# Performance work log

Measured on AMD Instinct MI355X. Metric: run time of the kernel, lower is better.

The kernel has to match this reference:

```python
import jax, jax.numpy as jnp
import numpy as np
from jax import lax

# ---- static config (matches init_kwargs) ----
B, D, H, HD, MLP = 64, 768, 12, 64, 3072
DEPTH = 11                     # trunk blocks; block 12 is used (twice) as b1/b2
IMG_H, IMG_W, P, S = 256, 128, 16, 12
NY, NX = (IMG_H - P) // S + 1, (IMG_W - P) // S + 1   # 21, 10
NP = NY * NX                   # 210 patches
N = NP + 1                     # +CLS = 211 tokens
NUM_CIDS = 8
SCALE = HD ** -0.5
SIE = 3.0                      # sie_xishu
SHIFT, GROUPS, DIV = 5, 2, 4
EPS = 1e-6
_PNAMES = ["ln1_g", "ln1_b", "qkv_w", "qkv_b", "proj_w", "proj_b",
           "ln2_g", "ln2_b", "fc1_w", "fc1_b", "fc2_w", "fc2_b"]


def layernorm(x, g, b):
    m = jnp.mean(x, -1, keepdims=True)
    v = jnp.mean(jnp.square(x - m), -1, keepdims=True)
    return (x - m) * lax.rsqrt(v + EPS) * g + b


def block(x, p):
    """Pre-norm ViT block: manual attention (q@k.T softmax @v) + GELU MLP."""
    ln1g, ln1b, qkvw, qkvb, projw, projb, ln2g, ln2b, fc1w, fc1b, fc2w, fc2b = p
    Bn, Nn = x.shape[0], x.shape[1]
    h = layernorm(x, ln1g, ln1b)
    qkv = (h @ qkvw + qkvb).reshape(Bn, Nn, 3, H, HD)
    q, k, v = qkv[:, :, 0], qkv[:, :, 1], qkv[:, :, 2]           # [B,N,H,HD]
    attn = jax.nn.softmax(jnp.einsum('bnhd,bmhd->bhnm', q * SCALE, k), axis=-1)
    o = jnp.einsum('bhnm,bmhd->bnhd', attn, v).reshape(Bn, Nn, D)
    x = x + o @ projw + projb
    h = layernorm(x, ln2g, ln2b)
    return x + jax.nn.gelu(h @ fc1w + fc1b, approximate=False) @ fc2w + fc2b


def _block_params(k, lead=()):
    ks = jax.random.split(k, 4)
    z = lambda s: jnp.zeros(lead + s, jnp.float32)
    o = lambda s: jnp.ones(lead + s, jnp.float32)
    r = lambda kk, s, fan: jax.random.normal(kk, lead + s, jnp.float32) * (fan ** -0.5)
    return dict(ln1_g=o((D,)), ln1_b=z((D,)),
                qkv_w=r(ks[0], (D, 3 * D), D), qkv_b=z((3 * D,)),
                proj_w=r(ks[1], (D, D), D), proj_b=z((D,)),
                ln2_g=o((D,)), ln2_b=z((D,)),
                fc1_w=r(ks[2], (D, MLP), D), fc1_b=z((MLP,)),
                fc2_w=r(ks[3], (MLP, D), MLP), fc2_b=z((D,)))


def setup_inputs() -> dict:
    key = jax.random.key(0)
    k = jax.random.split(key, 8)
    inp = {
        "x": jax.random.normal(k[0], (B, 3, IMG_H, IMG_W), jnp.float32),
        "cids": jax.random.randint(k[1], (B,), 0, NUM_CIDS),
        "conv_w": jax.random.normal(k[2], (D, 3, P, P), jnp.float32) * np.float32(np.sqrt(2.0 / (P * P * D))),
        "conv_b": jnp.zeros((D,), jnp.float32),
        "cls_token": jax.random.normal(k[3], (1, 1, D), jnp.float32) * 0.02,
        "pos_embed": jax.random.normal(k[4], (1, N, D), jnp.float32) * 0.02,
        "sie_embed": jax.random.normal(k[5], (NUM_CIDS, 1, D), jnp.float32) * 0.02,
    }
    for name, arr in _block_params(k[6], (DEPTH,)).items():
        inp["blk_" + name] = arr
    for pre, kk in (("b1_", jax.random.fold_in(key, 101)), ("b2_", jax.random.fold_in(key, 102))):
        for name, arr in _block_params(kk).items():
            inp[pre + name] = arr
        inp[pre + "norm_g"] = jnp.ones((D,), jnp.float32)
        inp[pre + "norm_b"] = jnp.zeros((D,), jnp.float32)
    return inp


def reference(x, cids, conv_w, conv_b, cls_token, pos_embed, sie_embed,
              blk_ln1_g, blk_ln1_b, blk_qkv_w, blk_qkv_b, blk_proj_w, blk_proj_b,
              blk_ln2_g, blk_ln2_b, blk_fc1_w, blk_fc1_b, blk_fc2_w, blk_fc2_b,
              b1_ln1_g, b1_ln1_b, b1_qkv_w, b1_qkv_b, b1_proj_w, b1_proj_b,
              b1_ln2_g, b1_ln2_b, b1_fc1_w, b1_fc1_b, b1_fc2_w, b1_fc2_b,
              b1_norm_g, b1_norm_b,
              b2_ln1_g, b2_ln1_b, b2_qkv_w, b2_qkv_b, b2_proj_w, b2_proj_b,
              b2_ln2_g, b2_ln2_b, b2_fc1_w, b2_fc1_b, b2_fc2_w, b2_fc2_b,
              b2_norm_g, b2_norm_b):
    Bn = x.shape[0]
    # overlapping patch embed: Conv2d(3->768, k=16, s=12), flatten, transpose
    y = lax.conv_general_dilated(x, conv_w, (S, S), 'VALID',
                                 dimension_numbers=('NCHW', 'OIHW', 'NCHW'))
    y = (y + conv_b[None, :, None, None]).reshape(Bn, D, NP).transpose(0, 2, 1)
    t = jnp.concatenate([jnp.broadcast_to(cls_token, (Bn, 1, D)), y], axis=1)
    t = t + pos_embed + SIE * sie_embed[cids]   # SIE camera embedding
    # 11 trunk blocks via scan over stacked params
    stk = (blk_ln1_g, blk_ln1_b, blk_qkv_w, blk_qkv_b, blk_proj_w, blk_proj_b,
           blk_ln2_g, blk_ln2_b, blk_fc1_w, blk_fc1_b, blk_fc2_w, blk_fc2_b)
    t = lax.scan(lambda c, p: (block(c, p), None), t, stk)[0]
    # global branch: b1 = block12 + final norm, take CLS
    b1p = (b1_ln1_g, b1_ln1_b, b1_qkv_w, b1_qkv_b, b1_proj_w, b1_proj_b,
           b1_ln2_g, b1_ln2_b, b1_fc1_w, b1_fc1_b, b1_fc2_w, b1_fc2_b)
    f0 = layernorm(block(t, b1p), b1_norm_g, b1_norm_b)[:, 0]
    # shuffle_unit(t, shift=5, group=2, begin=1) -> jigsaw rearranged patches [B,210,D]
    xs = jnp.concatenate([t[:, SHIFT:], t[:, 1:SHIFT]], axis=1)
    xs = xs.reshape(Bn, GROUPS, -1, D).transpose(0, 2, 1, 3).reshape(Bn, -1, D)
    token = t[:, 0:1]
    pl = NP // DIV                                   # 52
    b2p = (b2_ln1_g, b2_ln1_b, b2_qkv_w, b2_qkv_b, b2_proj_w, b2_proj_b,
           b2_ln2_g, b2_ln2_b, b2_fc1_w, b2_fc1_b, b2_fc2_w, b2_fc2_b)
    feats = [f0]
    for i in range(DIV):
        seg = jnp.concatenate([token, xs[:, i * pl:(i + 1) * pl]], axis=1)   # [B,53,D]
        feats.append(layernorm(block(seg, b2p), b2_norm_g, b2_norm_b)[:, 0])
    # eval output with neck_feat='before': necks pass features through;
    # concat global + local/divide_length -> [B, 5*768]
    return jnp.concatenate([feats[0]] + [f / DIV for f in feats[1:]], axis=1)
```

## Files before the change

kernel.cpp:

```cpp
#include <hip/hip_runtime.h>
#include <hip/hip_bf16.h>
#include <cstdint>
#include <cstddef>
#include <math.h>

using bf16 = __hip_bfloat16;
typedef __bf16 bf16x8 __attribute__((ext_vector_type(8)));
typedef float f32x4 __attribute__((ext_vector_type(4)));

static constexpr int NHEAD = 12;
static constexpr int NTOK  = 211;
static constexpr int DEPTH = 11;

static __device__ __forceinline__ void gload_lds16(const bf16* g, bf16* lds) {
  __builtin_amdgcn_global_load_lds(
      (const __attribute__((address_space(1))) uint32_t*)g,
      (__attribute__((address_space(3))) uint32_t*)lds,
      16, 0, 0);
}

__device__ __forceinline__ float gelu_f(float x) {
  float u = x * (0.7978845608f + 0.0356774081f * x * x);
  float t = 1.f - 2.f / (__expf(2.f * u) + 1.f);
  return 0.5f * x * (1.f + t);
}

static __device__ __forceinline__ unsigned short bf16_bits(float x) {
  return __builtin_bit_cast(unsigned short, __float2bfloat16(x));
}

template <bool GELU, bool RES, typename CT, int OUT>
__global__ __launch_bounds__(256) void gemm_db(
    const bf16* __restrict__ A, const bf16* __restrict__ Bt,
    const float* __restrict__ bias, const float* __restrict__ res,
    CT* __restrict__ C, int M, int N, int K, int gn, int sA, int sR, int sC,
    bf16* __restrict__ qh, bf16* __restrict__ kh, bf16* __restrict__ vh,
    int pad, int ntd, int coff)
{
  __shared__ bf16 sb[2][8192];

  const int tid = threadIdx.x;
  const int w = tid >> 6, l = tid & 63;
  const int lr = l & 15, lg = l >> 4;
  const int wr = (w >> 1) * 64, wc = (w & 1) * 64;

  const int nwg = gridDim.x, lin = blockIdx.x;
  const int q = nwg >> 3, r = nwg & 7;
  const int xcd = lin & 7, pos = lin >> 3;
  const int wg = (xcd < r ? xcd * (q + 1) : r * (q + 1) + (xcd - r) * q) + pos;
  const int bm0 = (wg / gn) * 128, bn0 = (wg % gn) * 128;

  f32x4 acc[4][4];
#pragma unroll
  for (int i = 0; i < 4; ++i)
#pragma unroll
    for (int j = 0; j < 4; ++j) acc[i][j] = f32x4{0.f, 0.f, 0.f, 0.f};

  size_t aof[2], bof[2]; int dst[2];
#pragma unroll
  for (int j = 0; j < 2; ++j) {
    const int c = j * 256 + tid;
    const int row = c >> 2;
    const int ch = (c & 3) ^ ((row >> 1) & 3);
    int ar = bm0 + row; if (ar >= M) ar = M - 1;
    aof[j] = (size_t)ar * sA + ch * 8;
    bof[j] = (size_t)(bn0 + row) * K + ch * 8;
    dst[j] = c * 8;
  }

  const int nt = K >> 5;

  auto stage = [&](int t) {
    bf16* s = sb[t & 1];
    const size_t ko = (size_t)t * 32;
    gload_lds16(A + aof[0] + ko, s + dst[0]);
    gload_lds16(A + aof[1] + ko, s + dst[1]);
    gload_lds16(Bt + bof[0] + ko, s + 4096 + dst[0]);
    gload_lds16(Bt + bof[1] + ko, s + 4096 + dst[1]);
  };

  stage(0);
  __syncthreads();

  const int swz = (lg ^ ((lr >> 1) & 3)) * 8;

  for (int t = 0; t < nt; ++t) {
    if (t + 1 < nt) stage(t + 1);
    const bf16* As = sb[t & 1];
    const bf16* Bs = As + 4096;
    bf16x8 af[4], bv[4];
#pragma unroll
    for (int mi = 0; mi < 4; ++mi)
      af[mi] = *(const bf16x8*)(As + (wr + mi * 16 + lr) * 32 + swz);
#pragma unroll
    for (int ni = 0; ni < 4; ++ni)
      bv[ni] = *(const bf16x8*)(Bs + (wc + ni * 16 + lr) * 32 + swz);
#pragma unroll
    for (int mi = 0; mi < 4; ++mi)
#pragma unroll
      for (int ni = 0; ni < 4; ++ni)
        acc[mi][ni] = __builtin_amdgcn_mfma_f32_16x16x32_bf16(af[mi], bv[ni], acc[mi][ni], 0, 0, 0);
    __syncthreads();
  }

  if constexpr (OUT == 2 || sizeof(CT) == 2) {
    char* lb = (char*)sb;
#pragma unroll
    for (int mi = 0; mi < 4; ++mi) {
#pragma unroll
      for (int ni = 0; ni < 4; ++ni) {
        const int cloc = wc + ni * 16 + lr;
        const float bvl = bias[bn0 + cloc];
#pragma unroll
        for (int r2 = 0; r2 < 4; ++r2) {
          const int rowl = wr + mi * 16 + lg * 4 + r2;
          float v = acc[mi][ni][r2] + bvl;
          if constexpr (GELU) v = gelu_f(v);
          *(unsigned short*)(lb + rowl * 256 + ((cloc * 2) ^ (((rowl >> 1) & 6) << 4))) =
              bf16_bits(v);
        }
      }
    }
    __syncthreads();
#pragma unroll
    for (int j = 0; j < 8; ++j) {
      const int flat = j * 256 + tid;
      const int row = flat >> 4, ch = flat & 15;
      const int grow = bm0 + row;
      if (grow < M) {
        const f32x4 v = *(const f32x4*)(lb + row * 256 + ((ch * 16) ^ (((row >> 1) & 6) << 4)));
        if constexpr (OUT == 2) {
          const int col0 = bn0 + ch * 8 + coff;
          const int region = (col0 >= 1536) ? 2 : (col0 >= 768 ? 1 : 0);
          const int c7 = col0 - region * 768;
          const int h = c7 >> 6, d = c7 & 63;
          const int bb2 = grow / ntd;
          const int tok = grow - bb2 * ntd;
          bf16* db = (region == 0) ? qh : ((region == 1) ? kh : vh);
          *(f32x4*)((char*)db + (((size_t)(bb2 * 12 + h) * pad + tok) * 64 + d) * 2) = v;
        } else {
          *(f32x4*)((char*)C + ((size_t)grow * sC + bn0 + ch * 8) * 2) = v;
        }
      }
    }
  } else {
#pragma unroll
    for (int mi = 0; mi < 4; ++mi) {
#pragma unroll
      for (int ni = 0; ni < 4; ++ni) {
        const int col = bn0 + wc + ni * 16 + lr;
        const float bvl = bias[col];
#pragma unroll
        for (int r2 = 0; r2 < 4; ++r2) {
          const int row = bm0 + wr + mi * 16 + lg * 4 + r2;
          if (row < M) {
            float v = acc[mi][ni][r2] + bvl;
            if constexpr (GELU) v = gelu_f(v);
            if constexpr (RES) v += res[(size_t)row * sR + col];
            C[(size_t)row * sC + col] = v;
          }
        }
      }
    }
  }
}

__global__ __launch_bounds__(256) void vtrans_kernel(
    const bf16* __restrict__ vcomp, bf16* __restrict__ vT, int ntok, int pad)
{
  __shared__ unsigned short t[224 * 65];
  const int bb = blockIdx.x, h = blockIdx.y;
  const unsigned short* src = (const unsigned short*)vcomp + (size_t)(bb * 12 + h) * pad * 64;
  for (int idx = threadIdx.x; idx < ntok * 64; idx += 256) {
    int tok = idx >> 6, d = idx & 63;
    t[tok * 65 + d] = src[idx];
  }
  __syncthreads();
  unsigned short* dstp = (unsigned short*)vT + (size_t)(bb * 12 + h) * 64 * pad;
  for (int idx = threadIdx.x; idx < 64 * ntok; idx += 256) {
    int d = idx / ntok, tok = idx - d * ntok;
    dstp[(size_t)d * pad + tok] = t[tok * 65 + d];
  }
}

template <int NKF, bool ONLY0>
__global__ __launch_bounds__(256) void attn_kernel(
    const bf16* __restrict__ qb, const bf16* __restrict__ kb,
    const bf16* __restrict__ vsrc, bf16* __restrict__ ao, int ntok, int pad)
{
  constexpr int NPAD = NKF * 16;
  constexpr int VST = NPAD + 8;
  __shared__ bf16 Pl[4][16][NPAD];
  __shared__ __bf16 Vt[ONLY0 ? 1 : 64][ONLY0 ? 1 : VST];
  const int bb = blockIdx.x;
  const int h = blockIdx.y;
  const int tid = threadIdx.x;
  const int w = tid >> 6, l = tid & 63;
  const int lr = l & 15, lg = l >> 4;
  const int bbh = bb * 12 + h;
  const __bf16* qbase = reinterpret_cast<const __bf16*>(qb) + (size_t)bbh * pad * 64;
  const __bf16* kbase = reinterpret_cast<const __bf16*>(kb) + (size_t)bbh * pad * 64;
  const __bf16* vglob = reinterpret_cast<const __bf16*>(vsrc) +
                        (ONLY0 ? (size_t)bbh * 64 * pad : (size_t)bbh * pad * 64);

  if constexpr (!ONLY0) {
    for (int idx = tid; idx < ntok * 64; idx += 256) {
      const int tok = idx >> 6, d = idx & 63;
      Vt[d][tok] = vglob[idx];
    }
    __syncthreads();
  }
  if (ONLY0 && w > 0) return;

  for (int qt = w; qt < (ONLY0 ? 1 : NKF); qt += 4) {
    int qrow = qt * 16 + lr; if (qrow >= ntok) qrow = ntok - 1;
    const __bf16* qp = qbase + qrow * 64 + lg * 8;
    const bf16x8 qf0 = *reinterpret_cast<const bf16x8*>(qp);
    const bf16x8 qf1 = *reinterpret_cast<const bf16x8*>(qp + 32);

    f32x4 s[NKF];
#pragma unroll
    for (int kf = 0; kf < NKF; ++kf) {
      int krow = kf * 16 + lr; if (krow >= ntok) krow = ntok - 1;
      const __bf16* kp = kbase + krow * 64 + lg * 8;
      f32x4 a = f32x4{0.f, 0.f, 0.f, 0.f};
      a = __builtin_amdgcn_mfma_f32_16x16x32_bf16(qf0, *reinterpret_cast<const bf16x8*>(kp), a, 0, 0, 0);
      a = __builtin_amdgcn_mfma_f32_16x16x32_bf16(qf1, *reinterpret_cast<const bf16x8*>(kp + 32), a, 0, 0, 0);
      s[kf] = a;
    }

    float rs[4];
#pragma unroll
    for (int r = 0; r < 4; ++r) {
      float mx = -1e30f;
#pragma unroll
      for (int kf = 0; kf < NKF; ++kf)
        if (kf * 16 + lr < ntok) mx = fmaxf(mx, s[kf][r]);
#pragma unroll
      for (int d = 1; d < 16; d <<= 1) mx = fmaxf(mx, __shfl_xor(mx, d));
      float sum = 0.f;
#pragma unroll
      for (int kf = 0; kf < NKF; ++kf) {
        float p = 0.f;
        if (kf * 16 + lr < ntok) p = __expf((s[kf][r] - mx) * 0.125f);
        sum += p;
        Pl[w][lg * 4 + r][kf * 16 + lr] = __float2bfloat16(p);
      }
#pragma unroll
      for (int d = 1; d < 16; d <<= 1) sum += __shfl_xor(sum, d);
      rs[r] = sum;
    }
    __builtin_amdgcn_s_waitcnt(0);

    f32x4 o[4];
#pragma unroll
    for (int ni = 0; ni < 4; ++ni) o[ni] = f32x4{0.f, 0.f, 0.f, 0.f};
#pragma unroll
    for (int ks = 0; ks < NPAD / 32; ++ks) {
      const bf16x8 pa = *reinterpret_cast<const bf16x8*>(&Pl[w][lr][ks * 32 + lg * 8]);
#pragma unroll
      for (int ni = 0; ni < 4; ++ni) {
        bf16x8 vb;
        if constexpr (ONLY0) {
          vb = *reinterpret_cast<const bf16x8*>(
              vglob + (size_t)(ni * 16 + lr) * pad + ks * 32 + lg * 8);
        } else {
          vb = *reinterpret_cast<const bf16x8*>(&Vt[ni * 16 + lr][ks * 32 + lg * 8]);
        }
        o[ni] = __builtin_amdgcn_mfma_f32_16x16x32_bf16(pa, vb, o[ni], 0, 0, 0);
      }
    }
#pragma unroll
    for (int ni = 0; ni < 4; ++ni)
#pragma unroll
      for (int r = 0; r < 4; ++r) {
        int qq = qt * 16 + lg * 4 + r;
        if (qq < (ONLY0 ? 1 : ntok)) {
          float val = o[ni][r] / rs[r];
          ao[((size_t)bb * ntok + qq) * 768 + h * 64 + ni * 16 + lr] = __float2bfloat16(val);
        }
      }
  }
}

static __device__ __forceinline__ void ln_row(
    const float* __restrict__ x, const float* __restrict__ g, const float* __restrict__ b,
    bf16* __restrict__ out, int row, int l)
{
  const float4* xr = reinterpret_cast<const float4*>(x + (size_t)row * 768);
  float4 v[3]; float s = 0.f;
#pragma unroll
  for (int i = 0; i < 3; ++i) {
    v[i] = xr[l + i * 64];
    s += v[i].x + v[i].y + v[i].z + v[i].w;
  }
#pragma unroll
  for (int d = 1; d < 64; d <<= 1) s += __shfl_xor(s, d);
  float mean = s * (1.f / 768.f);
  float s2 = 0.f;
#pragma unroll
  for (int i = 0; i < 3; ++i) {
    float a0 = v[i].x - mean, a1 = v[i].y - mean, a2 = v[i].z - mean, a3 = v[i].w - mean;
    s2 += a0 * a0 + a1 * a1 + a2 * a2 + a3 * a3;
  }
#pragma unroll
  for (int d = 1; d < 64; d <<= 1) s2 += __shfl_xor(s2, d);
  float rstd = rsqrtf(s2 * (1.f / 768.f) + 1e-6f);
  const float4* g4 = reinterpret_cast<const float4*>(g);
  const float4* b4 = reinterpret_cast<const float4*>(b);
  unsigned short* orow = reinterpret_cast<unsigned short*>(out + (size_t)row * 768);
#pragma unroll
  for (int i = 0; i < 3; ++i) {
    float4 gg = g4[l + i * 64], bb = b4[l + i * 64];
    ushort4 pk;
    pk.x = bf16_bits((v[i].x - mean) * rstd * gg.x + bb.x);
    pk.y = bf16_bits((v[i].y - mean) * rstd * gg.y + bb.y);
    pk.z = bf16_bits((v[i].z - mean) * rstd * gg.z + bb.z);
    pk.w = bf16_bits((v[i].w - mean) * rstd * gg.w + bb.w);
    *reinterpret_cast<ushort4*>(orow + (l + i * 64) * 4) = pk;
  }
}

__global__ __launch_bounds__(256) void ln_kernel(
    const float* __restrict__ x, const float* __restrict__ g, const float* __restrict__ b,
    bf16* __restrict__ out, int Mrows)
{
  int row = blockIdx.x * 4 + (threadIdx.x >> 6);
  if (row >= Mrows) return;
  ln_row(x, g, b, out, row, threadIdx.x & 63);
}

__global__ __launch_bounds__(256) void tln_kernel(
    const float* __restrict__ w0, const float* __restrict__ w1,
    const float* __restrict__ w2, const float* __restrict__ w3,
    bf16* __restrict__ d0, bf16* __restrict__ d1,
    bf16* __restrict__ d2, bf16* __restrict__ d3,
    const float* __restrict__ x, const float* __restrict__ g,
    const float* __restrict__ b, bf16* __restrict__ outh, int Mrows)
{
  __shared__ float tile[32][33];
  int id = blockIdx.x;
  if (id >= 6912) {
    int row = (id - 6912) * 4 + (threadIdx.x >> 6);
    if (row < Mrows) ln_row(x, g, b, outh, row, threadIdx.x & 63);
    return;
  }
  const float* in; bf16* out; int R, C, tt;
  if (id < 1728)      { in = w0; out = d0; R = 768;  C = 2304; tt = id; }
  else if (id < 2304) { in = w1; out = d1; R = 768;  C = 768;  tt = id - 1728; }
  else if (id < 4608) { in = w2; out = d2; R = 768;  C = 3072; tt = id - 2304; }
  else                { in = w3; out = d3; R = 3072; C = 768;  tt = id - 4608; }
  const int tc = C >> 5;
  int c0 = (tt % tc) * 32, r0 = (tt / tc) * 32;
  int tx = threadIdx.x & 31, ty = threadIdx.x >> 5;
#pragma unroll
  for (int i = 0; i < 4; ++i) {
    int rr = ty + i * 8;
    tile[rr][tx] = in[(size_t)(r0 + rr) * C + c0 + tx];
  }
  __syncthreads();
#pragma unroll
  for (int i = 0; i < 4; ++i) {
    int c = ty + i * 8;
    out[(size_t)(c0 + c) * R + r0 + tx] = __float2bfloat16(tile[tx][c]);
  }
}

__global__ __launch_bounds__(256) void ln_head_kernel(
    const float* __restrict__ x, int tokstride, const float* __restrict__ g,
    const float* __restrict__ b, float* __restrict__ out, int nbb, int mode)
{
  int bb = blockIdx.x * 4 + (threadIdx.x >> 6);
  if (bb >= nbb) return;
  int l = threadIdx.x & 63;
  const float* xr = x + (size_t)bb * tokstride * 768;
  float v[12]; float s = 0.f;
#pragma unroll
  for (int i = 0; i < 12; ++i) { v[i] = xr[l + i * 64]; s += v[i]; }
#pragma unroll
  for (int d = 1; d < 64; d <<= 1) s += __shfl_xor(s, d);
  float mean = s * (1.f / 768.f);
  float s2 = 0.f;
#pragma unroll
  for (int i = 0; i < 12; ++i) { float t = v[i] - mean; s2 += t * t; }
#pragma unroll
  for (int d = 1; d < 64; d <<= 1) s2 += __shfl_xor(s2, d);
  float rstd = rsqrtf(s2 * (1.f / 768.f) + 1e-6f);
  float scale = mode ? 0.25f : 1.f;
  int b_ = mode ? (bb & 63) : bb;
  int off = mode ? (1 + (bb >> 6)) * 768 : 0;
  float* orow = out + (size_t)b_ * 3840 + off;
#pragma unroll
  for (int i = 0; i < 12; ++i) {
    orow[l + i * 64] = ((v[i] - mean) * rstd * g[l + i * 64] + b[l + i * 64]) * scale;
  }
}

__global__ void prep_kernel(const float* __restrict__ x, bf16* __restrict__ pm,
                            const float* __restrict__ convw, bf16* __restrict__ cw)
{
  int idx = blockIdx.x * 256 + threadIdx.x;
  if (idx < 13440 * 768) {
    int k = idx % 768;
    int m = idx / 768;
    int b = m / 210, p = m % 210;
    int py = p / 10, px = p % 10;
    int c = k >> 8, ij = k & 255, i = ij >> 4, j = ij & 15;
    pm[idx] = __float2bfloat16(x[(((size_t)b * 3 + c) * 256 + py * 12 + i) * 128 + px * 12 + j]);
  } else {
    int idx2 = idx - 13440 * 768;
    if (idx2 < 768 * 768) cw[idx2] = __float2bfloat16(convw[idx2]);
  }
}

__global__ void assemble_kernel(
    const bf16* __restrict__ y, const float* __restrict__ cls, const float* __restrict__ pos,
    const float* __restrict__ sie, const int* __restrict__ cids, float* __restrict__ tA)
{
  int idx = blockIdx.x * 256 + threadIdx.x;
  if (idx >= 13504 * 768) return;
  int d = idx % 768;
  int t = (idx / 768) % 211;
  int b = idx / (768 * 211);
  float v = pos[t * 768 + d] + 3.0f * sie[cids[b] * 768 + d];
  if (t == 0) v += cls[d];
  else v += __bfloat162float(y[((size_t)b * 210 + (t - 1)) * 768 + d]);
  tA[idx] = v;
}

__global__ void gather_kernel(const float* __restrict__ tA, float* __restrict__ tB)
{
  int idx = blockIdx.x * 256 + threadIdx.x;
  if (idx >= 256 * 53 * 768) return;
  int d = idx % 768;
  int jj = (idx / 768) % 53;
  int bb = idx / (768 * 53);
  int i = bb >> 6, b = bb & 63;
  int src;
  if (jj == 0) src = 0;
  else {
    int jx = i * 52 + (jj - 1);
    int mm = (jx & 1) * 105 + (jx >> 1);
    src = (mm < 206) ? (5 + mm) : (1 + (mm - 206));
  }
  tB[idx] = tA[((size_t)b * 211 + src) * 768 + d];
}

struct BlkP {
  const float *ln1_g, *ln1_b, *qkv_w, *qkv_b, *proj_w, *proj_b;
  const float *ln2_g, *ln2_b, *fc1_w, *fc1_b, *fc2_w, *fc2_b;
};

extern "C" void kernel_launch(void* const* d_in, const int* in_sizes, int n_in,
                              void* d_out, int out_size, void* d_ws, size_t ws_size,
                              hipStream_t stream)
{
  (void)in_sizes; (void)n_in; (void)out_size; (void)ws_size;
  const float* xin   = (const float*)d_in[0];
  const int*   cids  = (const int*)  d_in[1];
  const float* convw = (const float*)d_in[2];
  const float* convb = (const float*)d_in[3];
  const float* cls   = (const float*)d_in[4];
  const float* pos   = (const float*)d_in[5];
  const float* sie   = (const float*)d_in[6];
  float* out = (float*)d_out;

  char* ws = (char*)d_ws;
  bf16*  qkvT = (bf16*)(ws + 0);
  bf16*  projT = (bf16*)(ws + 3538944);
  bf16*  fc1T = (bf16*)(ws + 4718592);
  bf16*  fc2T = (bf16*)(ws + 9437184);
  float* tA   = (float*)(ws + 14155776);
  float* tB   = (float*)(ws + 55640064);
  bf16*  hb   = (bf16*)(ws + 97320960);
  bf16*  qb   = (bf16*)(ws + 118161408);
  bf16*  kb   = (bf16*)(ws + 143327232);
  bf16*  vb   = (bf16*)(ws + 168493056);
  bf16*  big  = (bf16*)(ws + 118161408);
  char*  sbuf = ws + 193658880;
  float* y0   = (float*)(sbuf);
  bf16*  hb0  = (bf16*)(sbuf + 786432);
  bf16*  big0 = (bf16*)(sbuf + 1179648);
  float* f0b  = (float*)(sbuf + 2752512);
  bf16*  ao   = (bf16*)(ws + 201523200);
  bf16*  vTb  = (bf16*)(ws + 222363648);

  dim3 blk(256);

  auto apply_block = [&](float* xbuf, const BlkP& p, int nb, int ntok_) {
    const int M = nb * ntok_;
    const int gm = (M + 127) / 128;
    const int pad = (ntok_ == NTOK) ? 224 : 64;
    tln_kernel<<<dim3(6912 + (M + 3) / 4), blk, 0, stream>>>(
        p.qkv_w, p.proj_w, p.fc1_w, p.fc2_w, qkvT, projT, fc1T, fc2T,
        xbuf, p.ln1_g, p.ln1_b, hb, M);
    gemm_db<false, false, bf16, 2><<<dim3(gm * 18), blk, 0, stream>>>(
        hb, qkvT, p.qkv_b, nullptr, (bf16*)nullptr, M, 2304, 768, 18, 768, 0, 0,
        qb, kb, vb, pad, ntok_, 0);
    attn_kernel<14, false><<<dim3(nb, NHEAD), blk, 0, stream>>>(qb, kb, vb, ao, ntok_, pad);
    gemm_db<false, true, float, 0><<<dim3(gm * 6), blk, 0, stream>>>(
        ao, projT, p.proj_b, xbuf, xbuf, M, 768, 768, 6, 768, 768, 768,
        nullptr, nullptr, nullptr, 0, 1, 0);
    ln_kernel<<<dim3((M + 3) / 4), blk, 0, stream>>>(xbuf, p.ln2_g, p.ln2_b, hb, M);
    gemm_db<true, false, bf16, 0><<<dim3(gm * 24), blk, 0, stream>>>(
        hb, fc1T, p.fc1_b, nullptr, big, M, 3072, 768, 24, 768, 3072, 3072,
        nullptr, nullptr, nullptr, 0, 1, 0);
    gemm_db<false, true, float, 0><<<dim3(gm * 6), blk, 0, stream>>>(
        big, fc2T, p.fc2_b, xbuf, xbuf, M, 768, 3072, 6, 3072, 768, 768,
        nullptr, nullptr, nullptr, 0, 1, 0);
  };

  auto apply_head_block = [&](const float* xsrc, const BlkP& p, int nb, int ntok_,
                              const float* ng, const float* nbias, int mode) {
    const int M = nb * ntok_;
    const int gm = (M + 127) / 128;
    const int gm0 = (nb + 127) / 128;
    const int pad = (ntok_ == NTOK) ? 224 : 64;
    const int ts = ntok_ * 768;
    tln_kernel<<<dim3(6912 + (M + 3) / 4), blk, 0, stream>>>(
        p.qkv_w, p.proj_w, p.fc1_w, p.fc2_w, qkvT, projT, fc1T, fc2T,
        xsrc, p.ln1_g, p.ln1_b, hb, M);
    gemm_db<false, false, bf16, 2><<<dim3(gm * 12), blk, 0, stream>>>(
        hb, qkvT + 768 * 768, p.qkv_b + 768, nullptr, (bf16*)nullptr,
        M, 1536, 768, 12, 768, 0, 0, qb, kb, vb, pad, ntok_, 768);
    gemm_db<false, false, bf16, 2><<<dim3(gm0 * 6), blk, 0, stream>>>(
        hb, qkvT, p.qkv_b, nullptr, (bf16*)nullptr,
        nb, 768, 768, 6, ntok_ * 768, 0, 0, qb, kb, vb, pad, 1, 0);
    vtrans_kernel<<<dim3(nb, NHEAD), blk, 0, stream>>>(vb, vTb, ntok_, pad);
    if (ntok_ == NTOK)
      attn_kernel<14, true><<<dim3(nb, NHEAD), blk, 0, stream>>>(qb, kb, vTb, ao, ntok_, pad);
    else
      attn_kernel<4, true><<<dim3(nb, NHEAD), blk, 0, stream>>>(qb, kb, vTb, ao, ntok_, pad);
    gemm_db<false, true, float, 0><<<dim3(gm0 * 6), blk, 0, stream>>>(
        ao, projT, p.proj_b, xsrc, y0, nb, 768, 768, 6, ts, ts, 768,
        nullptr, nullptr, nullptr, 0, 1, 0);
    ln_kernel<<<dim3((nb + 3) / 4), blk, 0, stream>>>(y0, p.ln2_g, p.ln2_b, hb0, nb);
    gemm_db<true, false, bf16, 0><<<dim3(gm0 * 24), blk, 0, stream>>>(
        hb0, fc1T, p.fc1_b, nullptr, big0, nb, 3072, 768, 24, 768, 3072, 3072,
        nullptr, nullptr, nullptr, 0, 1, 0);
    gemm_db<false, true, float, 0><<<dim3(gm0 * 6), blk, 0, stream>>>(
        big0, fc2T, p.fc2_b, y0, f0b, nb, 768, 3072, 6, 3072, 768, 768,
        nullptr, nullptr, nullptr, 0, 1, 0);
    ln_head_kernel<<<dim3((nb + 3) / 4), blk, 0, stream>>>(
        f0b, 1, ng, nbias, out, nb, mode);
  };

  {
    int total = 13440 * 768 + 768 * 768;
    prep_kernel<<<dim3((total + 255) / 256), blk, 0, stream>>>(xin, big, convw, qkvT);
    gemm_db<false, false, bf16, 0><<<dim3(105 * 6), blk, 0, stream>>>(
        big, qkvT, convb, nullptr, ao, 13440, 768, 768, 6, 768, 768, 768,
        nullptr, nullptr, nullptr, 0, 1, 0);
    total = 13504 * 768;
    assemble_kernel<<<dim3((total + 255) / 256), blk, 0, stream>>>(ao, cls, pos, sie, cids, tA);
  }

  const float* bp[12];
  for (int i = 0; i < 12; ++i) bp[i] = (const float*)d_in[7 + i];
  for (int dd = 0; dd < DEPTH; ++dd) {
    BlkP p;
    p.ln1_g = bp[0] + dd * 768;                p.ln1_b = bp[1] + dd * 768;
    p.qkv_w = bp[2] + (size_t)dd * 768 * 2304; p.qkv_b = bp[3] + dd * 2304;
    p.proj_w = bp[4] + (size_t)dd * 768 * 768; p.proj_b = bp[5] + dd * 768;
    p.ln2_g = bp[6] + dd * 768;                p.ln2_b = bp[7] + dd * 768;
    p.fc1_w = bp[8] + (size_t)dd * 768 * 3072; p.fc1_b = bp[9] + dd * 3072;
    p.fc2_w = bp[10] + (size_t)dd * 3072 * 768; p.fc2_b = bp[11] + dd * 768;
    apply_block(tA, p, 64, NTOK);
  }

  {
    BlkP p;
    p.ln1_g = (const float*)d_in[19]; p.ln1_b = (const float*)d_in[20];
    p.qkv_w = (const float*)d_in[21]; p.qkv_b = (const float*)d_in[22];
    p.proj_w = (const float*)d_in[23]; p.proj_b = (const float*)d_in[24];
    p.ln2_g = (const float*)d_in[25]; p.ln2_b = (const float*)d_in[26];
    p.fc1_w = (const float*)d_in[27]; p.fc1_b = (const float*)d_in[28];
    p.fc2_w = (const float*)d_in[29]; p.fc2_b = (const float*)d_in[30];
    apply_head_block(tA, p, 64, NTOK,
                     (const float*)d_in[31], (const float*)d_in[32], 0);
  }

  {
    int total = 256 * 53 * 768;
    gather_kernel<<<dim3((total + 255) / 256), blk, 0, stream>>>(tA, tB);
    BlkP p;
    p.ln1_g = (const float*)d_in[33]; p.ln1_b = (const float*)d_in[34];
    p.qkv_w = (const float*)d_in[35]; p.qkv_b = (const float*)d_in[36];
    p.proj_w = (const float*)d_in[37]; p.proj_b = (const float*)d_in[38];
    p.ln2_g = (const float*)d_in[39]; p.ln2_b = (const float*)d_in[40];
    p.fc1_w = (const float*)d_in[41]; p.fc1_b = (const float*)d_in[42];
    p.fc2_w = (const float*)d_in[43]; p.fc2_b = (const float*)d_in[44];
    apply_head_block(tB, p, 256, 53,
                     (const float*)d_in[45], (const float*)d_in[46], 1);
  }
}
```

Measured before the change: 4.886 ms.

## Fuse jigsaw gather into LN1 and stage float GEMM epilogue through LDS

The standalone gather kernel that copied the shuffled 256x53x768 token tensor is removed. The first LayerNorm of the local branch now reads source rows through an index remap, and a small copy of only the CLS residual rows is folded into the same launch. Separately, the float-output GEMM epilogue is staged through shared memory so bias, residual and stores use coalesced 16-byte vector accesses instead of scattered scalar ones. This adds two extra barriers per epilogue and relies on residual strides and pointers being 16-byte aligned.

```diff
diff --git a/kernel.cpp b/kernel.cpp
--- a/kernel.cpp
+++ b/kernel.cpp
@@ -27,6 +27,19 @@
 
 static __device__ __forceinline__ unsigned short bf16_bits(float x) {
   return __builtin_bit_cast(unsigned short, __float2bfloat16(x));
+}
+
+static __device__ __forceinline__ int b2src(int row) {
+  int bb = row / 53, jj = row - bb * 53;
+  int i = bb >> 6, b = bb & 63;
+  int src;
+  if (jj == 0) src = 0;
+  else {
+    int jx = i * 52 + (jj - 1);
+    int mm = (jx & 1) * 105 + (jx >> 1);
+    src = (mm < 206) ? (5 + mm) : (1 + (mm - 206));
+  }
+  return b * 211 + src;
 }
 
 template <bool GELU, bool RES, typename CT, int OUT>
@@ -144,23 +157,42 @@
       }
     }
   } else {
-#pragma unroll
-    for (int mi = 0; mi < 4; ++mi) {
-#pragma unroll
-      for (int ni = 0; ni < 4; ++ni) {
-        const int col = bn0 + wc + ni * 16 + lr;
-        const float bvl = bias[col];
-#pragma unroll
-        for (int r2 = 0; r2 < 4; ++r2) {
-          const int row = bm0 + wr + mi * 16 + lg * 4 + r2;
-          if (row < M) {
-            float v = acc[mi][ni][r2] + bvl;
-            if constexpr (GELU) v = gelu_f(v);
-            if constexpr (RES) v += res[(size_t)row * sR + col];
-            C[(size_t)row * sC + col] = v;
+    float* lb4 = (float*)sb;
+#pragma unroll
+    for (int hh = 0; hh < 2; ++hh) {
+      if ((w & 1) == hh) {
+#pragma unroll
+        for (int mi = 0; mi < 4; ++mi) {
+#pragma unroll
+          for (int ni = 0; ni < 4; ++ni) {
+            const int c64 = ni * 16 + lr;
+            const float bvl = bias[bn0 + hh * 64 + c64];
+#pragma unroll
+            for (int r2 = 0; r2 < 4; ++r2) {
+              const int rowl = wr + mi * 16 + lg * 4 + r2;
+              float v = acc[mi][ni][r2] + bvl;
+              if constexpr (GELU) v = gelu_f(v);
+              lb4[rowl * 64 + c64] = v;
+            }
           }
         }
       }
+      __syncthreads();
+#pragma unroll
+      for (int j = 0; j < 8; ++j) {
+        const int flat = j * 256 + tid;
+        const int row = flat >> 4, cc = flat & 15;
+        const int grow = bm0 + row;
+        if (grow < M) {
+          f32x4 v = *(const f32x4*)(lb4 + row * 64 + cc * 4);
+          const int col0 = bn0 + hh * 64 + cc * 4;
+          if constexpr (RES) {
+            v += *(const f32x4*)(res + (size_t)grow * sR + col0);
+          }
+          *(f32x4*)((float*)C + (size_t)grow * sC + col0) = v;
+        }
+      }
+      __syncthreads();
     }
   }
 }
@@ -283,11 +315,11 @@
   }
 }
 
-static __device__ __forceinline__ void ln_row(
-    const float* __restrict__ x, const float* __restrict__ g, const float* __restrict__ b,
-    bf16* __restrict__ out, int row, int l)
-{
-  const float4* xr = reinterpret_cast<const float4*>(x + (size_t)row * 768);
+static __device__ __forceinline__ void ln_row2(
+    const float* __restrict__ xrow, const float* __restrict__ g, const float* __restrict__ b,
+    bf16* __restrict__ outrow, int l)
+{
+  const float4* xr = reinterpret_cast<const float4*>(xrow);
   float4 v[3]; float s = 0.f;
 #pragma unroll
   for (int i = 0; i < 3; ++i) {
@@ -308,7 +340,7 @@
   float rstd = rsqrtf(s2 * (1.f / 768.f) + 1e-6f);
   const float4* g4 = reinterpret_cast<const float4*>(g);
   const float4* b4 = reinterpret_cast<const float4*>(b);
-  unsigned short* orow = reinterpret_cast<unsigned short*>(out + (size_t)row * 768);
+  unsigned short* orow = reinterpret_cast<unsigned short*>(outrow);
 #pragma unroll
   for (int i = 0; i < 3; ++i) {
     float4 gg = g4[l + i * 64], bb = b4[l + i * 64];
@@ -327,7 +359,7 @@
 {
   int row = blockIdx.x * 4 + (threadIdx.x >> 6);
   if (row >= Mrows) return;
-  ln_row(x, g, b, out, row, threadIdx.x & 63);
+  ln_row2(x + (size_t)row * 768, g, b, out + (size_t)row * 768, threadIdx.x & 63);
 }
 
 __global__ __launch_bounds__(256) void tln_kernel(
@@ -336,13 +368,30 @@
     bf16* __restrict__ d0, bf16* __restrict__ d1,
     bf16* __restrict__ d2, bf16* __restrict__ d3,
     const float* __restrict__ x, const float* __restrict__ g,
-    const float* __restrict__ b, bf16* __restrict__ outh, int Mrows)
+    const float* __restrict__ b, bf16* __restrict__ outh, int Mrows,
+    int gmode, float* __restrict__ rdst, int nr)
 {
   __shared__ float tile[32][33];
   int id = blockIdx.x;
   if (id >= 6912) {
-    int row = (id - 6912) * 4 + (threadIdx.x >> 6);
-    if (row < Mrows) ln_row(x, g, b, outh, row, threadIdx.x & 63);
+    const int lnb = (Mrows + 3) / 4;
+    int seg = id - 6912;
+    if (seg < lnb) {
+      int row = seg * 4 + (threadIdx.x >> 6);
+      if (row < Mrows) {
+        int srow = gmode ? b2src(row) : row;
+        ln_row2(x + (size_t)srow * 768, g, b, outh + (size_t)row * 768, threadIdx.x & 63);
+      }
+    } else {
+      int rr = (seg - lnb) * 4 + (threadIdx.x >> 6);
+      if (rr < nr) {
+        const int l = threadIdx.x & 63;
+        const float4* src4 = reinterpret_cast<const float4*>(x + (size_t)(rr & 63) * 211 * 768);
+        float4* dst4 = reinterpret_cast<float4*>(rdst + (size_t)rr * 768);
+#pragma unroll
+        for (int i = 0; i < 3; ++i) dst4[l + i * 64] = src4[l + i * 64];
+      }
+    }
     return;
   }
   const float* in; bf16* out; int R, C, tt;
@@ -428,24 +477,6 @@
   tA[idx] = v;
 }
 
-__global__ void gather_kernel(const float* __restrict__ tA, float* __restrict__ tB)
-{
-  int idx = blockIdx.x * 256 + threadIdx.x;
-  if (idx >= 256 * 53 * 768) return;
-  int d = idx % 768;
-  int jj = (idx / 768) % 53;
-  int bb = idx / (768 * 53);
-  int i = bb >> 6, b = bb & 63;
-  int src;
-  if (jj == 0) src = 0;
-  else {
-    int jx = i * 52 + (jj - 1);
-    int mm = (jx & 1) * 105 + (jx >> 1);
-    src = (mm < 206) ? (5 + mm) : (1 + (mm - 206));
-  }
-  tB[idx] = tA[((size_t)b * 211 + src) * 768 + d];
-}
-
 struct BlkP {
   const float *ln1_g, *ln1_b, *qkv_w, *qkv_b, *proj_w, *proj_b;
   const float *ln2_g, *ln2_b, *fc1_w, *fc1_b, *fc2_w, *fc2_b;
@@ -471,7 +502,7 @@
   bf16*  fc1T = (bf16*)(ws + 4718592);
   bf16*  fc2T = (bf16*)(ws + 9437184);
   float* tA   = (float*)(ws + 14155776);
-  float* tB   = (float*)(ws + 55640064);
+  float* rcb  = (float*)(ws + 55640064);
   bf16*  hb   = (bf16*)(ws + 97320960);
   bf16*  qb   = (bf16*)(ws + 118161408);
   bf16*  kb   = (bf16*)(ws + 143327232);
@@ -493,7 +524,7 @@
     const int pad = (ntok_ == NTOK) ? 224 : 64;
     tln_kernel<<<dim3(6912 + (M + 3) / 4), blk, 0, stream>>>(
         p.qkv_w, p.proj_w, p.fc1_w, p.fc2_w, qkvT, projT, fc1T, fc2T,
-        xbuf, p.ln1_g, p.ln1_b, hb, M);
+        xbuf, p.ln1_g, p.ln1_b, hb, M, 0, nullptr, 0);
     gemm_db<false, false, bf16, 2><<<dim3(gm * 18), blk, 0, stream>>>(
         hb, qkvT, p.qkv_b, nullptr, (bf16*)nullptr, M, 2304, 768, 18, 768, 0, 0,
         qb, kb, vb, pad, ntok_, 0);
@@ -511,15 +542,16 @@
   };
 
   auto apply_head_block = [&](const float* xsrc, const BlkP& p, int nb, int ntok_,
-                              const float* ng, const float* nbias, int mode) {
+                              const float* ng, const float* nbias, int mode,
+                              int gmode, const float* resp, int rstride) {
     const int M = nb * ntok_;
     const int gm = (M + 127) / 128;
     const int gm0 = (nb + 127) / 128;
     const int pad = (ntok_ == NTOK) ? 224 : 64;
-    const int ts = ntok_ * 768;
-    tln_kernel<<<dim3(6912 + (M + 3) / 4), blk, 0, stream>>>(
+    const int nr = gmode ? nb : 0;
+    tln_kernel<<<dim3(6912 + (M + 3) / 4 + (nr + 3) / 4), blk, 0, stream>>>(
         p.qkv_w, p.proj_w, p.fc1_w, p.fc2_w, qkvT, projT, fc1T, fc2T,
-        xsrc, p.ln1_g, p.ln1_b, hb, M);
+        xsrc, p.ln1_g, p.ln1_b, hb, M, gmode, rcb, nr);
     gemm_db<false, false, bf16, 2><<<dim3(gm * 12), blk, 0, stream>>>(
         hb, qkvT + 768 * 768, p.qkv_b + 768, nullptr, (bf16*)nullptr,
         M, 1536, 768, 12, 768, 0, 0, qb, kb, vb, pad, ntok_, 768);
@@ -532,7 +564,7 @@
     else
       attn_kernel<4, true><<<dim3(nb, NHEAD), blk, 0, stream>>>(qb, kb, vTb, ao, ntok_, pad);
     gemm_db<false, true, float, 0><<<dim3(gm0 * 6), blk, 0, stream>>>(
-        ao, projT, p.proj_b, xsrc, y0, nb, 768, 768, 6, ts, ts, 768,
+        ao, projT, p.proj_b, resp, y0, nb, 768, 768, 6, ntok_ * 768, rstride, 768,
         nullptr, nullptr, nullptr, 0, 1, 0);
     ln_kernel<<<dim3((nb + 3) / 4), blk, 0, stream>>>(y0, p.ln2_g, p.ln2_b, hb0, nb);
     gemm_db<true, false, bf16, 0><<<dim3(gm0 * 24), blk, 0, stream>>>(
@@ -577,12 +609,11 @@
     p.fc1_w = (const float*)d_in[27]; p.fc1_b = (const float*)d_in[28];
     p.fc2_w = (const float*)d_in[29]; p.fc2_b = (const float*)d_in[30];
     apply_head_block(tA, p, 64, NTOK,
-                     (const float*)d_in[31], (const float*)d_in[32], 0);
+                     (const float*)d_in[31], (const float*)d_in[32], 0,
+                     0, tA, NTOK * 768);
   }
 
   {
-    int total = 256 * 53 * 768;
-    gather_kernel<<<dim3((total + 255) / 256), blk, 0, stream>>>(tA, tB);
     BlkP p;
     p.ln1_g = (const float*)d_in[33]; p.ln1_b = (const float*)d_in[34];
     p.qkv_w = (const float*)d_in[35]; p.qkv_b = (const float*)d_in[36];
@@ -590,7 +621,8 @@
     p.ln2_g = (const float*)d_in[39]; p.ln2_b = (const float*)d_in[40];
     p.fc1_w = (const float*)d_in[41]; p.fc1_b = (const float*)d_in[42];
     p.fc2_w = (const float*)d_in[43]; p.fc2_b = (const float*)d_in[44];
-    apply_head_block(tB, p, 256, 53,
-                     (const float*)d_in[45], (const float*)d_in[46], 1);
-  }
-}
+    apply_head_block(tA, p, 256, 53,
+                     (const float*)d_in[45], (const float*)d_in[46], 1,
+                     1, rcb, 768);
+  }
+}
```

Result: slower. 5.136 ms (+5.1%).
